# Kernel optimization log

Hardware: AMD Instinct MI355X
Metric: run time of the kernel (lower is better)

Reference implementation:

```python
import jax, jax.numpy as jnp
import numpy as np

N, E = 50000, 800000
F_IN, F_H, H, F_OUT = 128, 16, 8, 64
NEG_SLOPE = 0.2
LN_EPS = 1e-5


def setup_inputs() -> dict:
    key = jax.random.key(0)
    ks = jax.random.split(key, 8)
    g = lambda k, shp, fan: (jax.random.normal(k, shp, jnp.float32) / np.sqrt(fan).astype(np.float32))
    return {
        "x": jax.random.normal(ks[0], (N, F_IN), jnp.float32),
        "edge_index": jax.random.randint(ks[1], (2, E), 0, N, jnp.int32),
        "Wl1": g(ks[2], (F_IN, H * F_H), F_IN),
        "Wr1": g(ks[3], (F_IN, H * F_H), F_IN),
        "att1": g(ks[4], (H, F_H), F_H),
        "bias1": jnp.zeros((H * F_H,), jnp.float32),
        "g1": jnp.ones((H * F_H,), jnp.float32),
        "b1": jnp.zeros((H * F_H,), jnp.float32),
        "Wl2": g(ks[5], (H * F_H, F_OUT), H * F_H),
        "Wr2": g(ks[6], (H * F_H, F_OUT), H * F_H),
        "att2": g(ks[7], (1, F_OUT), F_OUT),
        "bias2": jnp.zeros((F_OUT,), jnp.float32),
        "g2": jnp.ones((F_OUT,), jnp.float32),
        "b2": jnp.zeros((F_OUT,), jnp.float32),
    }


def gatv2_conv(x, edge_index, Wl, Wr, att, bias, concat):
    """PyG GATv2Conv (eval mode, dropout inactive).
    message m_e = leaky_relu(xl[src] + xr[dst]); alpha = softmax_dst(<m_e, att>);
    out_i = sum_{e: dst=i} alpha_e * xl[src_e]. Concat or mean over heads, + bias.
    """
    n = x.shape[0]
    h, c = att.shape
    src, dst = edge_index[0], edge_index[1]
    xl = (x @ Wl).reshape(n, h, c)  # source transform (lin_l)
    xr = (x @ Wr).reshape(n, h, c)  # target transform (lin_r)
    e = jax.nn.leaky_relu(xl[src] + xr[dst], NEG_SLOPE)  # [E,h,c]
    a = jnp.einsum("ehc,hc->eh", e, att)  # [E,h]
    # segment softmax over destination node
    m = jax.ops.segment_max(a, dst, num_segments=n)  # [n,h]
    m = jnp.where(jnp.isfinite(m), m, 0.0)  # isolated nodes -> -inf guard
    ea = jnp.exp(a - m[dst])
    s = jax.ops.segment_sum(ea, dst, num_segments=n)
    alpha = ea / (s[dst] + 1e-16)  # [E,h]
    out = jax.ops.segment_sum(xl[src] * alpha[..., None], dst, num_segments=n)  # [n,h,c]
    out = out.reshape(n, h * c) if concat else out.mean(axis=1)
    return out + bias


def layer_norm(x, gamma, beta):
    mu = x.mean(-1, keepdims=True)
    var = ((x - mu) ** 2).mean(-1, keepdims=True)
    return (x - mu) * jax.lax.rsqrt(var + LN_EPS) * gamma + beta


def reference(x, edge_index, Wl1, Wr1, att1, bias1, g1, b1,
              Wl2, Wr2, att2, bias2, g2, b2):
    h1 = gatv2_conv(x, edge_index, Wl1, Wr1, att1, bias1, concat=True)
    h1 = jax.nn.elu(layer_norm(h1, g1, b1))
    h2 = gatv2_conv(h1, edge_index, Wl2, Wr2, att2, bias2, concat=False)
    return layer_norm(h2, g2, b2)
```

## Files before the change

### kernel.cpp

```cpp
#include <hip/hip_runtime.h>
#include <hip/hip_bf16.h>
#include <math.h>

typedef short s16x8 __attribute__((ext_vector_type(8)));
typedef float f32x4 __attribute__((ext_vector_type(4)));
typedef float f32x2 __attribute__((ext_vector_type(2)));

__device__ __forceinline__ float bflo(unsigned u) { return __uint_as_float(u << 16); }
__device__ __forceinline__ float bfhi(unsigned u) { return __uint_as_float(u & 0xffff0000u); }
__device__ __forceinline__ unsigned short f2bf(float f) {
    __hip_bfloat16 h = __float2bfloat16(f);
    return __builtin_bit_cast(unsigned short, h);
}
__device__ __forceinline__ f32x4 mfma_bf16(s16x8 a, s16x8 b, f32x4 c) {
    asm("v_mfma_f32_16x16x32_bf16 %0, %1, %2, %0" : "+v"(c) : "v"(a), "v"(b));
    return c;
}
__device__ __forceinline__ f32x2 unpk2(unsigned u) { return (f32x2){bflo(u), bfhi(u)}; }
__device__ __forceinline__ f32x2 plrelu(f32x2 x) {
    return __builtin_elementwise_max(x, x * 0.2f);
}
template <int CTRL>
__device__ __forceinline__ float dpp_add(float v) {
    int y = __builtin_amdgcn_update_dpp(0, __builtin_bit_cast(int, v), CTRL, 0xf, 0xf, true);
    return v + __builtin_bit_cast(float, y);
}
__device__ __forceinline__ float red8(float p) {
    p = dpp_add<0xB1>(p); p = dpp_add<0x4E>(p); return dpp_add<0x141>(p);
}
__device__ __forceinline__ float red16(float p) {
    p = dpp_add<0xB1>(p); p = dpp_add<0x4E>(p);
    p = dpp_add<0x141>(p); return dpp_add<0x140>(p);
}

__global__ void prep_kernel(const float* __restrict__ Wl1, const float* __restrict__ Wr1,
                            const float* __restrict__ Wl2, const float* __restrict__ Wr2,
                            unsigned short* __restrict__ Wt1, unsigned short* __restrict__ Wt2,
                            int* __restrict__ deg, int n) {
    int idx = blockIdx.x * 256 + threadIdx.x;
    if (idx < 256 * 128) {
        int c = idx >> 7, k = idx & 127;
        float v = (c < 128) ? Wl1[k * 128 + c] : Wr1[k * 128 + (c - 128)];
        Wt1[idx] = f2bf(v);
    } else if (idx < 256 * 128 + 128 * 128) {
        int j = idx - 256 * 128;
        int c = j >> 7, k = j & 127;
        float v = (c < 64) ? Wl2[k * 64 + c] : Wr2[k * 64 + (c - 64)];
        Wt2[j] = f2bf(v);
    } else {
        int z = idx - (256 * 128 + 128 * 128);
        int i = z * 4;
        if (i + 3 < n) *reinterpret_cast<int4*>(&deg[i]) = make_int4(0, 0, 0, 0);
        else {
            if (i < n) deg[i] = 0;
            if (i + 1 < n) deg[i + 1] = 0;
            if (i + 2 < n) deg[i + 2] = 0;
        }
    }
}

__global__ __launch_bounds__(256) void degree_gemm_kernel(
    const int* __restrict__ dst, int* __restrict__ deg, int* __restrict__ rank, int E,
    int dblocks,
    const float* __restrict__ A, const unsigned short* __restrict__ Wt,
    unsigned short* __restrict__ Cl, unsigned short* __restrict__ Cr, int nrows) {
    __shared__ unsigned short As[64 * 128];
    if (blockIdx.x < (unsigned)dblocks) {
        int e = blockIdx.x * 256 + threadIdx.x;
        if (e < E) rank[e] = atomicAdd(&deg[dst[e]], 1);
        return;
    }
    constexpr int NOUT = 256, HALF = 128, CT = 4;
    int t = threadIdx.x, lane = t & 63, wave = t >> 6;
    int row_base = (blockIdx.x - dblocks) * 64;
    int rows_here = nrows - row_base;
    #pragma unroll
    for (int it = 0; it < 4; ++it) {
        int q = it * 256 + t;
        int r = q >> 4, c8 = q & 15;
        int su = r * 16 + (c8 ^ (r & 7));
        s16x8 v = {0, 0, 0, 0, 0, 0, 0, 0};
        if (r < rows_here) {
            const float4* g = reinterpret_cast<const float4*>(
                A + ((size_t)(row_base + r)) * 128 + c8 * 8);
            float4 v0 = g[0], v1 = g[1];
            union { s16x8 s; unsigned short u[8]; } pk;
            pk.u[0] = f2bf(v0.x); pk.u[1] = f2bf(v0.y);
            pk.u[2] = f2bf(v0.z); pk.u[3] = f2bf(v0.w);
            pk.u[4] = f2bf(v1.x); pk.u[5] = f2bf(v1.y);
            pk.u[6] = f2bf(v1.z); pk.u[7] = f2bf(v1.w);
            v = pk.s;
        }
        reinterpret_cast<s16x8*>(As)[su] = v;
    }
    __syncthreads();
    int m16 = lane & 15, kg = lane >> 4;
    int colw = wave * (NOUT / 4);
    s16x8 bfr[CT][4];
    const s16x8* Wt16 = reinterpret_cast<const s16x8*>(Wt);
    #pragma unroll
    for (int ct = 0; ct < CT; ++ct)
        #pragma unroll
        for (int ks = 0; ks < 4; ++ks)
            bfr[ct][ks] = Wt16[(size_t)(colw + ct * 16 + m16) * 16 + ks * 4 + kg];
    f32x4 acc[4][CT];
    #pragma unroll
    for (int rt = 0; rt < 4; ++rt)
        #pragma unroll
        for (int ct = 0; ct < CT; ++ct) acc[rt][ct] = (f32x4){0.f, 0.f, 0.f, 0.f};
    const s16x8* As16 = reinterpret_cast<const s16x8*>(As);
    int sw = m16 & 7;
    #pragma unroll
    for (int rt = 0; rt < 4; ++rt) {
        int abase = (rt * 16 + m16) * 16;
        #pragma unroll
        for (int ks = 0; ks < 4; ++ks) {
            s16x8 af = As16[abase + ((ks * 4 + kg) ^ sw)];
            #pragma unroll
            for (int ct = 0; ct < CT; ++ct)
                acc[rt][ct] = mfma_bf16(bfr[ct][ks], af, acc[rt][ct]);
        }
    }
    #pragma unroll
    for (int rt = 0; rt < 4; ++rt) {
        int row = row_base + rt * 16 + m16;
        if (row < nrows) {
            #pragma unroll
            for (int ct = 0; ct < CT; ++ct) {
                int n0 = colw + ct * 16 + kg * 4;
                unsigned short* Cp = (n0 < HALF) ? (Cl + n0) : (Cr + (n0 - HALF));
                ushort4 w4;
                w4.x = f2bf(acc[rt][ct][0]);
                w4.y = f2bf(acc[rt][ct][1]);
                w4.z = f2bf(acc[rt][ct][2]);
                w4.w = f2bf(acc[rt][ct][3]);
                *reinterpret_cast<ushort4*>(&Cp[(size_t)row * HALF]) = w4;
            }
        }
    }
}

__global__ __launch_bounds__(1024) void scan_part_kernel(const int* __restrict__ deg,
                                                         int* __restrict__ off,
                                                         int* __restrict__ bsum, int n) {
    __shared__ int wsum[16];
    int t = threadIdx.x, lane = t & 63, w = t >> 6;
    int i = blockIdx.x * 4096 + t * 4;
    int4 v = make_int4(0, 0, 0, 0);
    if (i + 3 < n) v = *reinterpret_cast<const int4*>(&deg[i]);
    else {
        if (i < n) v.x = deg[i];
        if (i + 1 < n) v.y = deg[i + 1];
        if (i + 2 < n) v.z = deg[i + 2];
    }
    int tsum = v.x + v.y + v.z + v.w;
    int x = tsum;
    #pragma unroll
    for (int d = 1; d < 64; d <<= 1) { int y = __shfl_up(x, d); if (lane >= d) x += y; }
    if (lane == 63) wsum[w] = x;
    __syncthreads();
    if (t < 16) {
        int y = wsum[t];
        #pragma unroll
        for (int d = 1; d < 16; d <<= 1) { int z = __shfl_up(y, d); if (t >= d) y += z; }
        wsum[t] = y;
    }
    __syncthreads();
    int excl = ((w == 0) ? 0 : wsum[w - 1]) + (x - tsum);
    if (i < n) off[i] = excl;
    if (i + 1 < n) off[i + 1] = excl + v.x;
    if (i + 2 < n) off[i + 2] = excl + v.x + v.y;
    if (i + 3 < n) off[i + 3] = excl + v.x + v.y + v.z;
    __syncthreads();
    if (t == 1023) bsum[blockIdx.x] = wsum[15];
}

__global__ __launch_bounds__(1024) void scan_add_kernel(int* __restrict__ off,
                                                        const int* __restrict__ bsum,
                                                        int nblk, int n) {
    int b = blockIdx.x;
    int base = 0;
    for (int j = 0; j < b; ++j) base += bsum[j];
    int i = b * 4096 + threadIdx.x * 4;
    if (i + 3 < n) {
        int4 v = *reinterpret_cast<const int4*>(&off[i]);
        v.x += base; v.y += base; v.z += base; v.w += base;
        *reinterpret_cast<int4*>(&off[i]) = v;
    } else {
        if (i < n) off[i] += base;
        if (i + 1 < n) off[i + 1] += base;
        if (i + 2 < n) off[i + 2] += base;
    }
    if (b == 0 && threadIdx.x == 0) {
        int tot = 0;
        for (int j = 0; j < nblk; ++j) tot += bsum[j];
        off[n] = tot;
    }
}

__global__ void scatter_kernel(const int* __restrict__ src, const int* __restrict__ dst,
                               const int* __restrict__ off, const int* __restrict__ rank,
                               int* __restrict__ ssrc, int E) {
    int e = blockIdx.x * blockDim.x + threadIdx.x;
    if (e < E) {
        int d = dst[e];
        ssrc[off[d] + rank[e]] = src[e];
    }
}

__global__ __launch_bounds__(256) void mfma_gemm128_kernel(
    const unsigned short* __restrict__ A, const unsigned short* __restrict__ Wt,
    unsigned short* __restrict__ Cl, unsigned short* __restrict__ Cr, int nrows) {
    constexpr int NOUT = 128, HALF = 64, CT = 2;
    __shared__ unsigned short As[64 * 128];
    int t = threadIdx.x, lane = t & 63, wave = t >> 6;
    int row_base = blockIdx.x * 64;
    int rows_here = nrows - row_base;
    #pragma unroll
    for (int it = 0; it < 4; ++it) {
        int q = it * 256 + t;
        int r = q >> 4, c8 = q & 15;
        int su = r * 16 + (c8 ^ (r & 7));
        s16x8 v = {0, 0, 0, 0, 0, 0, 0, 0};
        if (r < rows_here)
            v = *reinterpret_cast<const s16x8*>(A + ((size_t)(row_base + r)) * 128 + c8 * 8);
        reinterpret_cast<s16x8*>(As)[su] = v;
    }
    __syncthreads();
    int m16 = lane & 15, kg = lane >> 4;
    int colw = wave * (NOUT / 4);
    s16x8 bfr[CT][4];
    const s16x8* Wt16 = reinterpret_cast<const s16x8*>(Wt);
    #pragma unroll
    for (int ct = 0; ct < CT; ++ct)
        #pragma unroll
        for (int ks = 0; ks < 4; ++ks)
            bfr[ct][ks] = Wt16[(size_t)(colw + ct * 16 + m16) * 16 + ks * 4 + kg];
    f32x4 acc[4][CT];
    #pragma unroll
    for (int rt = 0; rt < 4; ++rt)
        #pragma unroll
        for (int ct = 0; ct < CT; ++ct) acc[rt][ct] = (f32x4){0.f, 0.f, 0.f, 0.f};
    const s16x8* As16 = reinterpret_cast<const s16x8*>(As);
    int sw = m16 & 7;
    #pragma unroll
    for (int rt = 0; rt < 4; ++rt) {
        int abase = (rt * 16 + m16) * 16;
        #pragma unroll
        for (int ks = 0; ks < 4; ++ks) {
            s16x8 af = As16[abase + ((ks * 4 + kg) ^ sw)];
            #pragma unroll
            for (int ct = 0; ct < CT; ++ct)
                acc[rt][ct] = mfma_bf16(bfr[ct][ks], af, acc[rt][ct]);
        }
    }
    #pragma unroll
    for (int rt = 0; rt < 4; ++rt) {
        int row = row_base + rt * 16 + m16;
        if (row < nrows) {
            #pragma unroll
            for (int ct = 0; ct < CT; ++ct) {
                int n0 = colw + ct * 16 + kg * 4;
                unsigned short* Cp = (n0 < HALF) ? (Cl + n0) : (Cr + (n0 - HALF));
                ushort4 w4;
                w4.x = f2bf(acc[rt][ct][0]);
                w4.y = f2bf(acc[rt][ct][1]);
                w4.z = f2bf(acc[rt][ct][2]);
                w4.w = f2bf(acc[rt][ct][3]);
                *reinterpret_cast<ushort4*>(&Cp[(size_t)row * HALF]) = w4;
            }
        }
    }
}

__global__ __launch_bounds__(64) void gat1_kernel(
    const unsigned short* __restrict__ xl, const unsigned short* __restrict__ xr,
    const int* __restrict__ off, const int* __restrict__ ssrc,
    const float* __restrict__ att, const float* __restrict__ bias,
    const float* __restrict__ gamma, const float* __restrict__ beta,
    unsigned short* __restrict__ out, int n) {
    int lane = threadIdx.x;
    int node = blockIdx.x;
    if (node >= n) return;
    int h = lane >> 3;
    int i0 = h * 16 + ((lane & 7) << 1);
    f32x2 xrp = unpk2(*reinterpret_cast<const unsigned*>(xr + (size_t)node * 128 + i0));
    f32x2 atp = {att[i0], att[i0 + 1]};
    float s = 0.f;
    f32x2 ac = {0.f, 0.f};
    int beg = off[node], end = off[node + 1];
    int i = beg;
    for (; i + 4 <= end; i += 4) {
        int e0 = ssrc[i], e1 = ssrc[i + 1], e2 = ssrc[i + 2], e3 = ssrc[i + 3];
        unsigned u0 = *reinterpret_cast<const unsigned*>(xl + (size_t)e0 * 128 + i0);
        unsigned u1 = *reinterpret_cast<const unsigned*>(xl + (size_t)e1 * 128 + i0);
        unsigned u2 = *reinterpret_cast<const unsigned*>(xl + (size_t)e2 * 128 + i0);
        unsigned u3 = *reinterpret_cast<const unsigned*>(xl + (size_t)e3 * 128 + i0);
        f32x2 x0 = unpk2(u0), x1 = unpk2(u1), x2 = unpk2(u2), x3 = unpk2(u3);
        f32x2 q0 = plrelu(x0 + xrp) * atp;
        f32x2 q1 = plrelu(x1 + xrp) * atp;
        f32x2 q2 = plrelu(x2 + xrp) * atp;
        f32x2 q3 = plrelu(x3 + xrp) * atp;
        float p0 = q0.x + q0.y, p1 = q1.x + q1.y;
        float p2 = q2.x + q2.y, p3 = q3.x + q3.y;
        p0 = dpp_add<0xB1>(p0); p1 = dpp_add<0xB1>(p1);
        p2 = dpp_add<0xB1>(p2); p3 = dpp_add<0xB1>(p3);
        p0 = dpp_add<0x4E>(p0); p1 = dpp_add<0x4E>(p1);
        p2 = dpp_add<0x4E>(p2); p3 = dpp_add<0x4E>(p3);
        p0 = dpp_add<0x141>(p0); p1 = dpp_add<0x141>(p1);
        p2 = dpp_add<0x141>(p2); p3 = dpp_add<0x141>(p3);
        float w0 = __expf(fminf(p0, 60.f));
        float w1 = __expf(fminf(p1, 60.f));
        float w2 = __expf(fminf(p2, 60.f));
        float w3 = __expf(fminf(p3, 60.f));
        s += (w0 + w1) + (w2 + w3);
        ac += w0 * x0 + w1 * x1;
        ac += w2 * x2 + w3 * x3;
    }
    for (; i < end; ++i) {
        int e = ssrc[i];
        f32x2 xv = unpk2(*reinterpret_cast<const unsigned*>(xl + (size_t)e * 128 + i0));
        f32x2 q = plrelu(xv + xrp) * atp;
        float p = red8(q.x + q.y);
        float w = __expf(fminf(p, 60.f));
        s += w; ac += w * xv;
    }
    float inv = 1.f / (s + 1e-16f);
    float o0 = ac.x * inv + bias[i0];
    float o1 = ac.y * inv + bias[i0 + 1];
    float tsum = o0 + o1;
    #pragma unroll
    for (int d = 1; d < 64; d <<= 1) tsum += __shfl_xor(tsum, d);
    float mu = tsum * (1.f / 128.f);
    float d0 = o0 - mu, d1 = o1 - mu;
    float vsum = d0 * d0 + d1 * d1;
    #pragma unroll
    for (int d = 1; d < 64; d <<= 1) vsum += __shfl_xor(vsum, d);
    float rs = rsqrtf(vsum * (1.f / 128.f) + 1e-5f);
    float y0 = d0 * rs * gamma[i0] + beta[i0];
    float y1 = d1 * rs * gamma[i0 + 1] + beta[i0 + 1];
    y0 = y0 > 0.f ? y0 : expm1f(y0);
    y1 = y1 > 0.f ? y1 : expm1f(y1);
    unsigned pk = (unsigned)f2bf(y0) | ((unsigned)f2bf(y1) << 16);
    *reinterpret_cast<unsigned*>(out + (size_t)node * 128 + i0) = pk;
}

__global__ __launch_bounds__(64) void gat2_kernel(
    const unsigned short* __restrict__ xl, const unsigned short* __restrict__ xr,
    const int* __restrict__ off, const int* __restrict__ ssrc,
    const float* __restrict__ att, const float* __restrict__ bias,
    const float* __restrict__ gamma, const float* __restrict__ beta,
    float* __restrict__ out, int n) {
    int lane = threadIdx.x;
    int node = blockIdx.x;
    if (node >= n) return;
    int j2 = lane >> 4;
    int q = lane & 15;
    int fb = q * 4;
    uint2 uxr = *reinterpret_cast<const uint2*>(xr + (size_t)node * 64 + fb);
    f32x2 xr0 = unpk2(uxr.x), xr1 = unpk2(uxr.y);
    float4 at = *reinterpret_cast<const float4*>(att + fb);
    f32x2 at0 = {at.x, at.y}, at1 = {at.z, at.w};
    float s = 0.f;
    f32x2 ac0 = {0.f, 0.f}, ac1 = {0.f, 0.f};
    int beg = off[node], end = off[node + 1];
    for (int base = beg; base < end; base += 4) {
        int idx = base + j2;
        bool valid = idx < end;
        int e = ssrc[valid ? idx : beg];
        uint2 u = *reinterpret_cast<const uint2*>(xl + (size_t)e * 64 + fb);
        f32x2 x0 = unpk2(u.x), x1 = unpk2(u.y);
        f32x2 g0 = plrelu(x0 + xr0) * at0;
        f32x2 g1 = plrelu(x1 + xr1) * at1;
        f32x2 gs = g0 + g1;
        float p = red16(gs.x + gs.y);
        float w = valid ? __expf(fminf(p, 60.f)) : 0.f;
        s += w;
        ac0 += w * x0;
        ac1 += w * x1;
    }
    #pragma unroll
    for (int d = 16; d <= 32; d <<= 1) {
        s += __shfl_xor(s, d);
        ac0.x += __shfl_xor(ac0.x, d); ac0.y += __shfl_xor(ac0.y, d);
        ac1.x += __shfl_xor(ac1.x, d); ac1.y += __shfl_xor(ac1.y, d);
    }
    float inv = 1.f / (s + 1e-16f);
    float4 bi = *reinterpret_cast<const float4*>(bias + fb);
    float o0 = ac0.x * inv + bi.x;
    float o1 = ac0.y * inv + bi.y;
    float o2 = ac1.x * inv + bi.z;
    float o3 = ac1.y * inv + bi.w;
    float tsum = red16((o0 + o1) + (o2 + o3));
    float mu = tsum * (1.f / 64.f);
    float d0 = o0 - mu, d1 = o1 - mu, d2 = o2 - mu, d3 = o3 - mu;
    float vs = red16((d0 * d0 + d1 * d1) + (d2 * d2 + d3 * d3));
    float rs = rsqrtf(vs * (1.f / 64.f) + 1e-5f);
    if (j2 == 0) {
        float4 ga = *reinterpret_cast<const float4*>(gamma + fb);
        float4 be = *reinterpret_cast<const float4*>(beta + fb);
        float4 y;
        y.x = d0 * rs * ga.x + be.x;
        y.y = d1 * rs * ga.y + be.y;
        y.z = d2 * rs * ga.z + be.z;
        y.w = d3 * rs * ga.w + be.w;
        *reinterpret_cast<float4*>(out + (size_t)node * 64 + fb) = y;
    }
}

extern "C" void kernel_launch(void* const* d_in, const int* in_sizes, int n_in,
                              void* d_out, int out_size, void* d_ws, size_t ws_size,
                              hipStream_t stream) {
    const float* x = (const float*)d_in[0];
    const int* ei = (const int*)d_in[1];
    const float* Wl1 = (const float*)d_in[2];
    const float* Wr1 = (const float*)d_in[3];
    const float* att1 = (const float*)d_in[4];
    const float* bias1 = (const float*)d_in[5];
    const float* g1 = (const float*)d_in[6];
    const float* b1 = (const float*)d_in[7];
    const float* Wl2 = (const float*)d_in[8];
    const float* Wr2 = (const float*)d_in[9];
    const float* att2 = (const float*)d_in[10];
    const float* bias2 = (const float*)d_in[11];
    const float* g2 = (const float*)d_in[12];
    const float* b2 = (const float*)d_in[13];
    float* out = (float*)d_out;

    const int N = in_sizes[0] / 128;
    const int E = in_sizes[1] / 2;
    const int* src = ei;
    const int* dstp = ei + E;

    char* p = (char*)d_ws;
    auto alloc = [&](size_t bytes) -> char* {
        char* r = p;
        p += (bytes + 255) & ~(size_t)255;
        return r;
    };
    int* deg = (int*)alloc((size_t)N * 4);
    int* rank = (int*)alloc((size_t)E * 4);
    int* off = (int*)alloc((size_t)(N + 1) * 4);
    int* ssrc = (int*)alloc((size_t)E * 4);
    int* bsum = (int*)alloc(64 * 4);
    unsigned short* Wt1 = (unsigned short*)alloc(256 * 128 * 2);
    unsigned short* Wt2 = (unsigned short*)alloc(128 * 128 * 2);
    unsigned short* bufA = (unsigned short*)alloc((size_t)N * 128 * 2);
    unsigned short* bufB = (unsigned short*)alloc((size_t)N * 128 * 2);
    unsigned short* h1u = (unsigned short*)alloc((size_t)N * 128 * 2);

    const int nblk = (N + 4095) / 4096;
    const int gblocks = (N + 63) / 64;
    const int dblocks = (E + 255) / 256;
    const int prep_threads = 256 * 128 + 128 * 128 + (N + 3) / 4;

    prep_kernel<<<(prep_threads + 255) / 256, 256, 0, stream>>>(
        Wl1, Wr1, Wl2, Wr2, Wt1, Wt2, deg, N);
    degree_gemm_kernel<<<dblocks + gblocks, 256, 0, stream>>>(
        dstp, deg, rank, E, dblocks, x, Wt1, bufA, bufB, N);
    scan_part_kernel<<<nblk, 1024, 0, stream>>>(deg, off, bsum, N);
    scan_add_kernel<<<nblk, 1024, 0, stream>>>(off, bsum, nblk, N);
    scatter_kernel<<<(E + 255) / 256, 256, 0, stream>>>(src, dstp, off, rank, ssrc, E);
    gat1_kernel<<<N, 64, 0, stream>>>(bufA, bufB, off, ssrc, att1, bias1, g1, b1, h1u, N);
    mfma_gemm128_kernel<<<gblocks, 256, 0, stream>>>(h1u, Wt2, bufA, bufB, N);
    gat2_kernel<<<N, 64, 0, stream>>>(bufA, bufB, off, ssrc, att2, bias2, g2, b2, out, N);
}
```

Before: 252.9 us.

## Fuse layer-1 GAT aggregation with layer-2 MFMA projection via shared memory

```diff
diff --git a/kernel.cpp b/kernel.cpp
--- a/kernel.cpp
+++ b/kernel.cpp
@@ -208,141 +208,119 @@
     }
 }
 
-__global__ __launch_bounds__(256) void mfma_gemm128_kernel(
-    const unsigned short* __restrict__ A, const unsigned short* __restrict__ Wt,
-    unsigned short* __restrict__ Cl, unsigned short* __restrict__ Cr, int nrows) {
-    constexpr int NOUT = 128, HALF = 64, CT = 2;
-    __shared__ unsigned short As[64 * 128];
-    int t = threadIdx.x, lane = t & 63, wave = t >> 6;
-    int row_base = blockIdx.x * 64;
-    int rows_here = nrows - row_base;
-    #pragma unroll
-    for (int it = 0; it < 4; ++it) {
-        int q = it * 256 + t;
-        int r = q >> 4, c8 = q & 15;
-        int su = r * 16 + (c8 ^ (r & 7));
-        s16x8 v = {0, 0, 0, 0, 0, 0, 0, 0};
-        if (r < rows_here)
-            v = *reinterpret_cast<const s16x8*>(A + ((size_t)(row_base + r)) * 128 + c8 * 8);
-        reinterpret_cast<s16x8*>(As)[su] = v;
-    }
-    __syncthreads();
-    int m16 = lane & 15, kg = lane >> 4;
-    int colw = wave * (NOUT / 4);
-    s16x8 bfr[CT][4];
-    const s16x8* Wt16 = reinterpret_cast<const s16x8*>(Wt);
-    #pragma unroll
-    for (int ct = 0; ct < CT; ++ct)
-        #pragma unroll
-        for (int ks = 0; ks < 4; ++ks)
-            bfr[ct][ks] = Wt16[(size_t)(colw + ct * 16 + m16) * 16 + ks * 4 + kg];
-    f32x4 acc[4][CT];
-    #pragma unroll
-    for (int rt = 0; rt < 4; ++rt)
-        #pragma unroll
-        for (int ct = 0; ct < CT; ++ct) acc[rt][ct] = (f32x4){0.f, 0.f, 0.f, 0.f};
-    const s16x8* As16 = reinterpret_cast<const s16x8*>(As);
-    int sw = m16 & 7;
-    #pragma unroll
-    for (int rt = 0; rt < 4; ++rt) {
-        int abase = (rt * 16 + m16) * 16;
-        #pragma unroll
-        for (int ks = 0; ks < 4; ++ks) {
-            s16x8 af = As16[abase + ((ks * 4 + kg) ^ sw)];
-            #pragma unroll
-            for (int ct = 0; ct < CT; ++ct)
-                acc[rt][ct] = mfma_bf16(bfr[ct][ks], af, acc[rt][ct]);
-        }
-    }
-    #pragma unroll
-    for (int rt = 0; rt < 4; ++rt) {
-        int row = row_base + rt * 16 + m16;
-        if (row < nrows) {
-            #pragma unroll
-            for (int ct = 0; ct < CT; ++ct) {
-                int n0 = colw + ct * 16 + kg * 4;
-                unsigned short* Cp = (n0 < HALF) ? (Cl + n0) : (Cr + (n0 - HALF));
-                ushort4 w4;
-                w4.x = f2bf(acc[rt][ct][0]);
-                w4.y = f2bf(acc[rt][ct][1]);
-                w4.z = f2bf(acc[rt][ct][2]);
-                w4.w = f2bf(acc[rt][ct][3]);
-                *reinterpret_cast<ushort4*>(&Cp[(size_t)row * HALF]) = w4;
-            }
-        }
-    }
-}
-
-__global__ __launch_bounds__(64) void gat1_kernel(
+__global__ __launch_bounds__(256) void gat1_fused_kernel(
     const unsigned short* __restrict__ xl, const unsigned short* __restrict__ xr,
     const int* __restrict__ off, const int* __restrict__ ssrc,
     const float* __restrict__ att, const float* __restrict__ bias,
     const float* __restrict__ gamma, const float* __restrict__ beta,
-    unsigned short* __restrict__ out, int n) {
-    int lane = threadIdx.x;
-    int node = blockIdx.x;
-    if (node >= n) return;
+    const unsigned short* __restrict__ Wt2,
+    unsigned short* __restrict__ Cl, unsigned short* __restrict__ Cr, int n) {
+    __shared__ unsigned short Ys[16 * 128];
+    int t = threadIdx.x, lane = t & 63, wave = t >> 6;
+    int base = blockIdx.x * 16;
     int h = lane >> 3;
     int i0 = h * 16 + ((lane & 7) << 1);
-    f32x2 xrp = unpk2(*reinterpret_cast<const unsigned*>(xr + (size_t)node * 128 + i0));
-    f32x2 atp = {att[i0], att[i0 + 1]};
-    float s = 0.f;
-    f32x2 ac = {0.f, 0.f};
-    int beg = off[node], end = off[node + 1];
-    int i = beg;
-    for (; i + 4 <= end; i += 4) {
-        int e0 = ssrc[i], e1 = ssrc[i + 1], e2 = ssrc[i + 2], e3 = ssrc[i + 3];
-        unsigned u0 = *reinterpret_cast<const unsigned*>(xl + (size_t)e0 * 128 + i0);
-        unsigned u1 = *reinterpret_cast<const unsigned*>(xl + (size_t)e1 * 128 + i0);
-        unsigned u2 = *reinterpret_cast<const unsigned*>(xl + (size_t)e2 * 128 + i0);
-        unsigned u3 = *reinterpret_cast<const unsigned*>(xl + (size_t)e3 * 128 + i0);
-        f32x2 x0 = unpk2(u0), x1 = unpk2(u1), x2 = unpk2(u2), x3 = unpk2(u3);
-        f32x2 q0 = plrelu(x0 + xrp) * atp;
-        f32x2 q1 = plrelu(x1 + xrp) * atp;
-        f32x2 q2 = plrelu(x2 + xrp) * atp;
-        f32x2 q3 = plrelu(x3 + xrp) * atp;
-        float p0 = q0.x + q0.y, p1 = q1.x + q1.y;
-        float p2 = q2.x + q2.y, p3 = q3.x + q3.y;
-        p0 = dpp_add<0xB1>(p0); p1 = dpp_add<0xB1>(p1);
-        p2 = dpp_add<0xB1>(p2); p3 = dpp_add<0xB1>(p3);
-        p0 = dpp_add<0x4E>(p0); p1 = dpp_add<0x4E>(p1);
-        p2 = dpp_add<0x4E>(p2); p3 = dpp_add<0x4E>(p3);
-        p0 = dpp_add<0x141>(p0); p1 = dpp_add<0x141>(p1);
-        p2 = dpp_add<0x141>(p2); p3 = dpp_add<0x141>(p3);
-        float w0 = __expf(fminf(p0, 60.f));
-        float w1 = __expf(fminf(p1, 60.f));
-        float w2 = __expf(fminf(p2, 60.f));
-        float w3 = __expf(fminf(p3, 60.f));
-        s += (w0 + w1) + (w2 + w3);
-        ac += w0 * x0 + w1 * x1;
-        ac += w2 * x2 + w3 * x3;
-    }
-    for (; i < end; ++i) {
-        int e = ssrc[i];
-        f32x2 xv = unpk2(*reinterpret_cast<const unsigned*>(xl + (size_t)e * 128 + i0));
-        f32x2 q = plrelu(xv + xrp) * atp;
-        float p = red8(q.x + q.y);
-        float w = __expf(fminf(p, 60.f));
-        s += w; ac += w * xv;
-    }
-    float inv = 1.f / (s + 1e-16f);
-    float o0 = ac.x * inv + bias[i0];
-    float o1 = ac.y * inv + bias[i0 + 1];
-    float tsum = o0 + o1;
-    #pragma unroll
-    for (int d = 1; d < 64; d <<= 1) tsum += __shfl_xor(tsum, d);
-    float mu = tsum * (1.f / 128.f);
-    float d0 = o0 - mu, d1 = o1 - mu;
-    float vsum = d0 * d0 + d1 * d1;
-    #pragma unroll
-    for (int d = 1; d < 64; d <<= 1) vsum += __shfl_xor(vsum, d);
-    float rs = rsqrtf(vsum * (1.f / 128.f) + 1e-5f);
-    float y0 = d0 * rs * gamma[i0] + beta[i0];
-    float y1 = d1 * rs * gamma[i0 + 1] + beta[i0 + 1];
-    y0 = y0 > 0.f ? y0 : expm1f(y0);
-    y1 = y1 > 0.f ? y1 : expm1f(y1);
-    unsigned pk = (unsigned)f2bf(y0) | ((unsigned)f2bf(y1) << 16);
-    *reinterpret_cast<unsigned*>(out + (size_t)node * 128 + i0) = pk;
+    int u16 = i0 >> 3;
+    int dw = (i0 & 7) >> 1;
+    for (int q = 0; q < 4; ++q) {
+        int slot = wave * 4 + q;
+        int node = base + slot;
+        unsigned pk = 0;
+        if (node < n) {
+            f32x2 xrp = unpk2(*reinterpret_cast<const unsigned*>(xr + (size_t)node * 128 + i0));
+            f32x2 atp = {att[i0], att[i0 + 1]};
+            float s = 0.f;
+            f32x2 ac = {0.f, 0.f};
+            int beg = off[node], end = off[node + 1];
+            int i = beg;
+            for (; i + 4 <= end; i += 4) {
+                int e0 = ssrc[i], e1 = ssrc[i + 1], e2 = ssrc[i + 2], e3 = ssrc[i + 3];
+                unsigned u0 = *reinterpret_cast<const unsigned*>(xl + (size_t)e0 * 128 + i0);
+                unsigned u1 = *reinterpret_cast<const unsigned*>(xl + (size_t)e1 * 128 + i0);
+                unsigned u2 = *reinterpret_cast<const unsigned*>(xl + (size_t)e2 * 128 + i0);
+                unsigned u3 = *reinterpret_cast<const unsigned*>(xl + (size_t)e3 * 128 + i0);
+                f32x2 x0 = unpk2(u0), x1 = unpk2(u1), x2 = unpk2(u2), x3 = unpk2(u3);
+                f32x2 q0 = plrelu(x0 + xrp) * atp;
+                f32x2 q1 = plrelu(x1 + xrp) * atp;
+                f32x2 q2 = plrelu(x2 + xrp) * atp;
+                f32x2 q3 = plrelu(x3 + xrp) * atp;
+                float p0 = q0.x + q0.y, p1 = q1.x + q1.y;
+                float p2 = q2.x + q2.y, p3 = q3.x + q3.y;
+                p0 = dpp_add<0xB1>(p0); p1 = dpp_add<0xB1>(p1);
+                p2 = dpp_add<0xB1>(p2); p3 = dpp_add<0xB1>(p3);
+                p0 = dpp_add<0x4E>(p0); p1 = dpp_add<0x4E>(p1);
+                p2 = dpp_add<0x4E>(p2); p3 = dpp_add<0x4E>(p3);
+                p0 = dpp_add<0x141>(p0); p1 = dpp_add<0x141>(p1);
+                p2 = dpp_add<0x141>(p2); p3 = dpp_add<0x141>(p3);
+                float w0 = __expf(fminf(p0, 60.f));
+                float w1 = __expf(fminf(p1, 60.f));
+                float w2 = __expf(fminf(p2, 60.f));
+                float w3 = __expf(fminf(p3, 60.f));
+                s += (w0 + w1) + (w2 + w3);
+                ac += w0 * x0 + w1 * x1;
+                ac += w2 * x2 + w3 * x3;
+            }
+            for (; i < end; ++i) {
+                int e = ssrc[i];
+                f32x2 xv = unpk2(*reinterpret_cast<const unsigned*>(xl + (size_t)e * 128 + i0));
+                f32x2 qv = plrelu(xv + xrp) * atp;
+                float p = red8(qv.x + qv.y);
+                float w = __expf(fminf(p, 60.f));
+                s += w; ac += w * xv;
+            }
+            float inv = 1.f / (s + 1e-16f);
+            float o0 = ac.x * inv + bias[i0];
+            float o1 = ac.y * inv + bias[i0 + 1];
+            float tsum = o0 + o1;
+            #pragma unroll
+            for (int d = 1; d < 64; d <<= 1) tsum += __shfl_xor(tsum, d);
+            float mu = tsum * (1.f / 128.f);
+            float d0 = o0 - mu, d1 = o1 - mu;
+            float vsum = d0 * d0 + d1 * d1;
+            #pragma unroll
+            for (int d = 1; d < 64; d <<= 1) vsum += __shfl_xor(vsum, d);
+            float rs = rsqrtf(vsum * (1.f / 128.f) + 1e-5f);
+            float y0 = d0 * rs * gamma[i0] + beta[i0];
+            float y1 = d1 * rs * gamma[i0 + 1] + beta[i0 + 1];
+            y0 = y0 > 0.f ? y0 : expm1f(y0);
+            y1 = y1 > 0.f ? y1 : expm1f(y1);
+            pk = (unsigned)f2bf(y0) | ((unsigned)f2bf(y1) << 16);
+        }
+        int su = u16 ^ (slot & 7);
+        *reinterpret_cast<unsigned*>(&Ys[(slot * 16 + su) * 8 + dw * 2]) = pk;
+    }
+    __syncthreads();
+    int m16 = lane & 15, kg = lane >> 4;
+    int colw = wave * 32;
+    const s16x8* Wt16 = reinterpret_cast<const s16x8*>(Wt2);
+    const s16x8* As16 = reinterpret_cast<const s16x8*>(Ys);
+    int sw = m16 & 7;
+    f32x4 acc[2];
+    acc[0] = (f32x4){0.f, 0.f, 0.f, 0.f};
+    acc[1] = (f32x4){0.f, 0.f, 0.f, 0.f};
+    #pragma unroll
+    for (int ks = 0; ks < 4; ++ks) {
+        s16x8 af = As16[m16 * 16 + ((ks * 4 + kg) ^ sw)];
+        #pragma unroll
+        for (int ct = 0; ct < 2; ++ct) {
+            s16x8 bf = Wt16[(size_t)(colw + ct * 16 + m16) * 16 + ks * 4 + kg];
+            acc[ct] = mfma_bf16(bf, af, acc[ct]);
+        }
+    }
+    int row = base + m16;
+    if (row < n) {
+        #pragma unroll
+        for (int ct = 0; ct < 2; ++ct) {
+            int n0 = colw + ct * 16 + kg * 4;
+            unsigned short* Cp = (n0 < 64) ? (Cl + n0) : (Cr + (n0 - 64));
+            ushort4 w4;
+            w4.x = f2bf(acc[ct][0]);
+            w4.y = f2bf(acc[ct][1]);
+            w4.z = f2bf(acc[ct][2]);
+            w4.w = f2bf(acc[ct][3]);
+            *reinterpret_cast<ushort4*>(&Cp[(size_t)row * 64]) = w4;
+        }
+    }
 }
 
 __global__ __launch_bounds__(64) void gat2_kernel(
@@ -447,7 +425,8 @@
     unsigned short* Wt2 = (unsigned short*)alloc(128 * 128 * 2);
     unsigned short* bufA = (unsigned short*)alloc((size_t)N * 128 * 2);
     unsigned short* bufB = (unsigned short*)alloc((size_t)N * 128 * 2);
-    unsigned short* h1u = (unsigned short*)alloc((size_t)N * 128 * 2);
+    unsigned short* bufC = (unsigned short*)alloc((size_t)N * 64 * 2);
+    unsigned short* bufD = (unsigned short*)alloc((size_t)N * 64 * 2);
 
     const int nblk = (N + 4095) / 4096;
     const int gblocks = (N + 63) / 64;
@@ -461,7 +440,7 @@
     scan_part_kernel<<<nblk, 1024, 0, stream>>>(deg, off, bsum, N);
     scan_add_kernel<<<nblk, 1024, 0, stream>>>(off, bsum, nblk, N);
     scatter_kernel<<<(E + 255) / 256, 256, 0, stream>>>(src, dstp, off, rank, ssrc, E);
-    gat1_kernel<<<N, 64, 0, stream>>>(bufA, bufB, off, ssrc, att1, bias1, g1, b1, h1u, N);
-    mfma_gemm128_kernel<<<gblocks, 256, 0, stream>>>(h1u, Wt2, bufA, bufB, N);
-    gat2_kernel<<<N, 64, 0, stream>>>(bufA, bufB, off, ssrc, att2, bias2, g2, b2, out, N);
-}
+    gat1_fused_kernel<<<(N + 15) / 16, 256, 0, stream>>>(
+        bufA, bufB, off, ssrc, att1, bias1, g1, b1, Wt2, bufC, bufD, N);
+    gat2_kernel<<<N, 64, 0, stream>>>(bufC, bufD, off, ssrc, att2, bias2, g2, b2, out, N);
+}
```

After: 264.6 us. 4.6% more time.

## Split degree counters into four sub-buckets to reduce atomic contention

Applied to the files above, without the earlier changes.

```diff
diff --git a/kernel.cpp b/kernel.cpp
--- a/kernel.cpp
+++ b/kernel.cpp
@@ -36,7 +36,7 @@
 __global__ void prep_kernel(const float* __restrict__ Wl1, const float* __restrict__ Wr1,
                             const float* __restrict__ Wl2, const float* __restrict__ Wr2,
                             unsigned short* __restrict__ Wt1, unsigned short* __restrict__ Wt2,
-                            int* __restrict__ deg, int n) {
+                            int* __restrict__ deg4, int n4) {
     int idx = blockIdx.x * 256 + threadIdx.x;
     if (idx < 256 * 128) {
         int c = idx >> 7, k = idx & 127;
@@ -50,24 +50,24 @@
     } else {
         int z = idx - (256 * 128 + 128 * 128);
         int i = z * 4;
-        if (i + 3 < n) *reinterpret_cast<int4*>(&deg[i]) = make_int4(0, 0, 0, 0);
+        if (i + 3 < n4) *reinterpret_cast<int4*>(&deg4[i]) = make_int4(0, 0, 0, 0);
         else {
-            if (i < n) deg[i] = 0;
-            if (i + 1 < n) deg[i + 1] = 0;
-            if (i + 2 < n) deg[i + 2] = 0;
+            if (i < n4) deg4[i] = 0;
+            if (i + 1 < n4) deg4[i + 1] = 0;
+            if (i + 2 < n4) deg4[i + 2] = 0;
         }
     }
 }
 
 __global__ __launch_bounds__(256) void degree_gemm_kernel(
-    const int* __restrict__ dst, int* __restrict__ deg, int* __restrict__ rank, int E,
-    int dblocks,
+    const int* __restrict__ dst, int* __restrict__ deg4, int* __restrict__ rank, int E,
+    int N, int dblocks,
     const float* __restrict__ A, const unsigned short* __restrict__ Wt,
     unsigned short* __restrict__ Cl, unsigned short* __restrict__ Cr, int nrows) {
     __shared__ unsigned short As[64 * 128];
     if (blockIdx.x < (unsigned)dblocks) {
         int e = blockIdx.x * 256 + threadIdx.x;
-        if (e < E) rank[e] = atomicAdd(&deg[dst[e]], 1);
+        if (e < E) rank[e] = atomicAdd(&deg4[(e & 3) * N + dst[e]], 1);
         return;
     }
     constexpr int NOUT = 256, HALF = 128, CT = 4;
@@ -140,19 +140,37 @@
     }
 }
 
-__global__ __launch_bounds__(1024) void scan_part_kernel(const int* __restrict__ deg,
+__global__ __launch_bounds__(1024) void scan_part_kernel(const int* __restrict__ deg4,
                                                          int* __restrict__ off,
-                                                         int* __restrict__ bsum, int n) {
+                                                         int4* __restrict__ sbase,
+                                                         int* __restrict__ bsum,
+                                                         int n, int N) {
     __shared__ int wsum[16];
     int t = threadIdx.x, lane = t & 63, w = t >> 6;
     int i = blockIdx.x * 4096 + t * 4;
-    int4 v = make_int4(0, 0, 0, 0);
-    if (i + 3 < n) v = *reinterpret_cast<const int4*>(&deg[i]);
-    else {
-        if (i < n) v.x = deg[i];
-        if (i + 1 < n) v.y = deg[i + 1];
-        if (i + 2 < n) v.z = deg[i + 2];
-    }
+    int4 A0 = make_int4(0, 0, 0, 0), A1 = A0, A2 = A0, A3 = A0;
+    if (i + 3 < n) {
+        A0 = *reinterpret_cast<const int4*>(&deg4[0 * N + i]);
+        A1 = *reinterpret_cast<const int4*>(&deg4[1 * N + i]);
+        A2 = *reinterpret_cast<const int4*>(&deg4[2 * N + i]);
+        A3 = *reinterpret_cast<const int4*>(&deg4[3 * N + i]);
+    } else {
+        int* a0 = &A0.x; int* a1 = &A1.x; int* a2 = &A2.x; int* a3 = &A3.x;
+        for (int j = 0; j < 4; ++j) {
+            if (i + j < n) {
+                a0[j] = deg4[0 * N + i + j];
+                a1[j] = deg4[1 * N + i + j];
+                a2[j] = deg4[2 * N + i + j];
+                a3[j] = deg4[3 * N + i + j];
+            }
+        }
+    }
+    int4 v = make_int4(A0.x + A1.x + A2.x + A3.x, A0.y + A1.y + A2.y + A3.y,
+                       A0.z + A1.z + A2.z + A3.z, A0.w + A1.w + A2.w + A3.w);
+    if (i < n) sbase[i] = make_int4(0, A0.x, A0.x + A1.x, A0.x + A1.x + A2.x);
+    if (i + 1 < n) sbase[i + 1] = make_int4(0, A0.y, A0.y + A1.y, A0.y + A1.y + A2.y);
+    if (i + 2 < n) sbase[i + 2] = make_int4(0, A0.z, A0.z + A1.z, A0.z + A1.z + A2.z);
+    if (i + 3 < n) sbase[i + 3] = make_int4(0, A0.w, A0.w + A1.w, A0.w + A1.w + A2.w);
     int tsum = v.x + v.y + v.z + v.w;
     int x = tsum;
     #pragma unroll
@@ -176,20 +194,28 @@
 }
 
 __global__ __launch_bounds__(1024) void scan_add_kernel(int* __restrict__ off,
+                                                        int4* __restrict__ sbase,
                                                         const int* __restrict__ bsum,
                                                         int nblk, int n) {
     int b = blockIdx.x;
     int base = 0;
     for (int j = 0; j < b; ++j) base += bsum[j];
     int i = b * 4096 + threadIdx.x * 4;
+    int o[4];
     if (i + 3 < n) {
         int4 v = *reinterpret_cast<const int4*>(&off[i]);
-        v.x += base; v.y += base; v.z += base; v.w += base;
-        *reinterpret_cast<int4*>(&off[i]) = v;
+        o[0] = v.x + base; o[1] = v.y + base; o[2] = v.z + base; o[3] = v.w + base;
+        *reinterpret_cast<int4*>(&off[i]) = make_int4(o[0], o[1], o[2], o[3]);
     } else {
-        if (i < n) off[i] += base;
-        if (i + 1 < n) off[i + 1] += base;
-        if (i + 2 < n) off[i + 2] += base;
+        for (int j = 0; j < 4; ++j)
+            if (i + j < n) { o[j] = off[i + j] + base; off[i + j] = o[j]; }
+    }
+    #pragma unroll
+    for (int j = 0; j < 4; ++j) {
+        if (i + j < n) {
+            int4 s = sbase[i + j];
+            sbase[i + j] = make_int4(s.x + o[j], s.y + o[j], s.z + o[j], s.w + o[j]);
+        }
     }
     if (b == 0 && threadIdx.x == 0) {
         int tot = 0;
@@ -199,12 +225,13 @@
 }
 
 __global__ void scatter_kernel(const int* __restrict__ src, const int* __restrict__ dst,
-                               const int* __restrict__ off, const int* __restrict__ rank,
+                               const int* __restrict__ abase, const int* __restrict__ rank,
                                int* __restrict__ ssrc, int E) {
     int e = blockIdx.x * blockDim.x + threadIdx.x;
     if (e < E) {
         int d = dst[e];
-        ssrc[off[d] + rank[e]] = src[e];
+        int pos = abase[4 * d + (e & 3)] + rank[e];
+        ssrc[pos] = src[e];
     }
 }
 
@@ -259,7 +286,7 @@
         int row = row_base + rt * 16 + m16;
         if (row < nrows) {
             #pragma unroll
-            for (int ct = 0; ct < CT; ++ct) {
+            for (int ct = 0; ct < 2; ++ct) {
                 int n0 = colw + ct * 16 + kg * 4;
                 unsigned short* Cp = (n0 < HALF) ? (Cl + n0) : (Cr + (n0 - HALF));
                 ushort4 w4;
@@ -438,9 +465,10 @@
         p += (bytes + 255) & ~(size_t)255;
         return r;
     };
-    int* deg = (int*)alloc((size_t)N * 4);
+    int* deg4 = (int*)alloc((size_t)N * 4 * 4);
     int* rank = (int*)alloc((size_t)E * 4);
     int* off = (int*)alloc((size_t)(N + 1) * 4);
+    int4* sbase = (int4*)alloc((size_t)N * 16);
     int* ssrc = (int*)alloc((size_t)E * 4);
     int* bsum = (int*)alloc(64 * 4);
     unsigned short* Wt1 = (unsigned short*)alloc(256 * 128 * 2);
@@ -452,15 +480,17 @@
     const int nblk = (N + 4095) / 4096;
     const int gblocks = (N + 63) / 64;
     const int dblocks = (E + 255) / 256;
-    const int prep_threads = 256 * 128 + 128 * 128 + (N + 3) / 4;
+    const int n4 = N * 4;
+    const int prep_threads = 256 * 128 + 128 * 128 + (n4 + 3) / 4;
 
     prep_kernel<<<(prep_threads + 255) / 256, 256, 0, stream>>>(
-        Wl1, Wr1, Wl2, Wr2, Wt1, Wt2, deg, N);
+        Wl1, Wr1, Wl2, Wr2, Wt1, Wt2, deg4, n4);
     degree_gemm_kernel<<<dblocks + gblocks, 256, 0, stream>>>(
-        dstp, deg, rank, E, dblocks, x, Wt1, bufA, bufB, N);
-    scan_part_kernel<<<nblk, 1024, 0, stream>>>(deg, off, bsum, N);
-    scan_add_kernel<<<nblk, 1024, 0, stream>>>(off, bsum, nblk, N);
-    scatter_kernel<<<(E + 255) / 256, 256, 0, stream>>>(src, dstp, off, rank, ssrc, E);
+        dstp, deg4, rank, E, N, dblocks, x, Wt1, bufA, bufB, N);
+    scan_part_kernel<<<nblk, 1024, 0, stream>>>(deg4, off, sbase, bsum, N, N);
+    scan_add_kernel<<<nblk, 1024, 0, stream>>>(off, sbase, bsum, nblk, N);
+    scatter_kernel<<<(E + 255) / 256, 256, 0, stream>>>(src, dstp, (const int*)sbase, rank,
+                                                        ssrc, E);
     gat1_kernel<<<N, 64, 0, stream>>>(bufA, bufB, off, ssrc, att1, bias1, g1, b1, h1u, N);
     mfma_gemm128_kernel<<<gblocks, 256, 0, stream>>>(h1u, Wt2, bufA, bufB, N);
     gat2_kernel<<<N, 64, 0, stream>>>(bufA, bufB, off, ssrc, att2, bias2, g2, b2, out, N);
```

Result: no change. 255.5 us (+1.0%).

## Build CSR via two-level bucket partition instead of atomic degree, scan and scatter

Applied to the files above, without the earlier changes.

```diff
diff --git a/kernel.cpp b/kernel.cpp
--- a/kernel.cpp
+++ b/kernel.cpp
@@ -33,10 +33,12 @@
     p = dpp_add<0x141>(p); return dpp_add<0x140>(p);
 }
 
+#define EPB 2048
+#define BSTRIDE 8192
+
 __global__ void prep_kernel(const float* __restrict__ Wl1, const float* __restrict__ Wr1,
                             const float* __restrict__ Wl2, const float* __restrict__ Wr2,
-                            unsigned short* __restrict__ Wt1, unsigned short* __restrict__ Wt2,
-                            int* __restrict__ deg, int n) {
+                            unsigned short* __restrict__ Wt1, unsigned short* __restrict__ Wt2) {
     int idx = blockIdx.x * 256 + threadIdx.x;
     if (idx < 256 * 128) {
         int c = idx >> 7, k = idx & 127;
@@ -47,32 +49,59 @@
         int c = j >> 7, k = j & 127;
         float v = (c < 64) ? Wl2[k * 64 + c] : Wr2[k * 64 + (c - 64)];
         Wt2[j] = f2bf(v);
-    } else {
-        int z = idx - (256 * 128 + 128 * 128);
-        int i = z * 4;
-        if (i + 3 < n) *reinterpret_cast<int4*>(&deg[i]) = make_int4(0, 0, 0, 0);
-        else {
-            if (i < n) deg[i] = 0;
-            if (i + 1 < n) deg[i + 1] = 0;
-            if (i + 2 < n) deg[i + 2] = 0;
-        }
-    }
-}
-
-__global__ __launch_bounds__(256) void degree_gemm_kernel(
-    const int* __restrict__ dst, int* __restrict__ deg, int* __restrict__ rank, int E,
-    int dblocks,
+    }
+}
+
+__global__ __launch_bounds__(256) void part_gemm_kernel(
+    const int* __restrict__ src, const int* __restrict__ dst, int* __restrict__ cnt,
+    int* __restrict__ bucketbuf, int E, int NB, int pblocks,
     const float* __restrict__ A, const unsigned short* __restrict__ Wt,
     unsigned short* __restrict__ Cl, unsigned short* __restrict__ Cr, int nrows) {
-    __shared__ unsigned short As[64 * 128];
-    if (blockIdx.x < (unsigned)dblocks) {
-        int e = blockIdx.x * 256 + threadIdx.x;
-        if (e < E) rank[e] = atomicAdd(&deg[dst[e]], 1);
+    __shared__ char smem[19456];
+    int t = threadIdx.x;
+    if (blockIdx.x < (unsigned)pblocks) {
+        int* sdst = (int*)smem;
+        int* ssl = (int*)(smem + 8192);
+        int* hist = (int*)(smem + 16384);
+        int* gbase = (int*)(smem + 17408);
+        int* cursor = (int*)(smem + 18432);
+        int e0 = blockIdx.x * EPB;
+        #pragma unroll
+        for (int it = 0; it < EPB / 256; ++it) {
+            int i = it * 256 + t;
+            int e = e0 + i;
+            sdst[i] = (e < E) ? dst[e] : -1;
+            ssl[i] = (e < E) ? src[e] : 0;
+        }
+        if (t < NB) hist[t] = 0;
+        __syncthreads();
+        #pragma unroll
+        for (int it = 0; it < EPB / 256; ++it) {
+            int d = sdst[it * 256 + t];
+            if (d >= 0) atomicAdd(&hist[d >> 8], 1);
+        }
+        __syncthreads();
+        if (t < NB) {
+            gbase[t] = atomicAdd(&cnt[t], hist[t]);
+            cursor[t] = 0;
+        }
+        __syncthreads();
+        #pragma unroll
+        for (int it = 0; it < EPB / 256; ++it) {
+            int i = it * 256 + t;
+            int d = sdst[i];
+            if (d >= 0) {
+                int b = d >> 8;
+                int l = atomicAdd(&cursor[b], 1);
+                bucketbuf[b * BSTRIDE + gbase[b] + l] = ((d & 255) << 16) | ssl[i];
+            }
+        }
         return;
     }
+    unsigned short* As = (unsigned short*)smem;
     constexpr int NOUT = 256, HALF = 128, CT = 4;
-    int t = threadIdx.x, lane = t & 63, wave = t >> 6;
-    int row_base = (blockIdx.x - dblocks) * 64;
+    int lane = t & 63, wave = t >> 6;
+    int row_base = (blockIdx.x - pblocks) * 64;
     int rows_here = nrows - row_base;
     #pragma unroll
     for (int it = 0; it < 4; ++it) {
@@ -140,71 +169,53 @@
     }
 }
 
-__global__ __launch_bounds__(1024) void scan_part_kernel(const int* __restrict__ deg,
-                                                         int* __restrict__ off,
-                                                         int* __restrict__ bsum, int n) {
-    __shared__ int wsum[16];
-    int t = threadIdx.x, lane = t & 63, w = t >> 6;
-    int i = blockIdx.x * 4096 + t * 4;
-    int4 v = make_int4(0, 0, 0, 0);
-    if (i + 3 < n) v = *reinterpret_cast<const int4*>(&deg[i]);
-    else {
-        if (i < n) v.x = deg[i];
-        if (i + 1 < n) v.y = deg[i + 1];
-        if (i + 2 < n) v.z = deg[i + 2];
-    }
-    int tsum = v.x + v.y + v.z + v.w;
-    int x = tsum;
-    #pragma unroll
-    for (int d = 1; d < 64; d <<= 1) { int y = __shfl_up(x, d); if (lane >= d) x += y; }
-    if (lane == 63) wsum[w] = x;
-    __syncthreads();
-    if (t < 16) {
-        int y = wsum[t];
-        #pragma unroll
-        for (int d = 1; d < 16; d <<= 1) { int z = __shfl_up(y, d); if (t >= d) y += z; }
-        wsum[t] = y;
-    }
-    __syncthreads();
-    int excl = ((w == 0) ? 0 : wsum[w - 1]) + (x - tsum);
-    if (i < n) off[i] = excl;
-    if (i + 1 < n) off[i + 1] = excl + v.x;
-    if (i + 2 < n) off[i + 2] = excl + v.x + v.y;
-    if (i + 3 < n) off[i + 3] = excl + v.x + v.y + v.z;
-    __syncthreads();
-    if (t == 1023) bsum[blockIdx.x] = wsum[15];
-}
-
-__global__ __launch_bounds__(1024) void scan_add_kernel(int* __restrict__ off,
-                                                        const int* __restrict__ bsum,
-                                                        int nblk, int n) {
-    int b = blockIdx.x;
-    int base = 0;
-    for (int j = 0; j < b; ++j) base += bsum[j];
-    int i = b * 4096 + threadIdx.x * 4;
-    if (i + 3 < n) {
-        int4 v = *reinterpret_cast<const int4*>(&off[i]);
-        v.x += base; v.y += base; v.z += base; v.w += base;
-        *reinterpret_cast<int4*>(&off[i]) = v;
-    } else {
-        if (i < n) off[i] += base;
-        if (i + 1 < n) off[i + 1] += base;
-        if (i + 2 < n) off[i + 2] += base;
-    }
-    if (b == 0 && threadIdx.x == 0) {
-        int tot = 0;
-        for (int j = 0; j < nblk; ++j) tot += bsum[j];
-        off[n] = tot;
-    }
-}
-
-__global__ void scatter_kernel(const int* __restrict__ src, const int* __restrict__ dst,
-                               const int* __restrict__ off, const int* __restrict__ rank,
-                               int* __restrict__ ssrc, int E) {
-    int e = blockIdx.x * blockDim.x + threadIdx.x;
-    if (e < E) {
-        int d = dst[e];
-        ssrc[off[d] + rank[e]] = src[e];
+__global__ __launch_bounds__(256) void bucket_csr_kernel(
+    const int* __restrict__ cnt, const int* __restrict__ bucketbuf,
+    int* __restrict__ off, int* __restrict__ ssrc, int N, int NB, int E) {
+    __shared__ int nhist[256];
+    __shared__ int ncur[256];
+    __shared__ int wred[4];
+    int b = blockIdx.x, t = threadIdx.x;
+    int lane = t & 63, wv = t >> 6;
+    int v = (t < b && t < NB) ? cnt[t] : 0;
+    float vf = __int_as_float(v);
+    (void)vf;
+    int x = v;
+    #pragma unroll
+    for (int d = 1; d < 64; d <<= 1) x += __shfl_xor(x, d);
+    if (lane == 0) wred[wv] = x;
+    __syncthreads();
+    int ebase = wred[0] + wred[1] + wred[2] + wred[3];
+    int ne = cnt[b];
+    int nb0 = b << 8;
+    int nn = min(256, N - nb0);
+    nhist[t] = 0;
+    __syncthreads();
+    const int* bb = bucketbuf + (size_t)b * BSTRIDE;
+    for (int i = t; i < ne; i += 256) {
+        int p = bb[i];
+        atomicAdd(&nhist[p >> 16], 1);
+    }
+    __syncthreads();
+    int h = nhist[t];
+    int sx = h;
+    #pragma unroll
+    for (int d = 1; d < 64; d <<= 1) { int y = __shfl_up(sx, d); if (lane >= d) sx += y; }
+    if (lane == 63) wred[wv] = sx;
+    __syncthreads();
+    int woff = 0;
+    #pragma unroll
+    for (int j = 0; j < 4; ++j) woff += (j < wv) ? wred[j] : 0;
+    int excl = woff + sx - h;
+    if (t < nn) off[nb0 + t] = ebase + excl;
+    ncur[t] = excl;
+    if (b == NB - 1 && t == 0) off[N] = ebase + ne;
+    __syncthreads();
+    for (int i = t; i < ne; i += 256) {
+        int p = bb[i];
+        int nl = p >> 16;
+        int l = atomicAdd(&ncur[nl], 1);
+        ssrc[ebase + l] = p & 0xFFFF;
     }
 }
 
@@ -259,7 +270,7 @@
         int row = row_base + rt * 16 + m16;
         if (row < nrows) {
             #pragma unroll
-            for (int ct = 0; ct < CT; ++ct) {
+            for (int ct = 0; ct < 2; ++ct) {
                 int n0 = colw + ct * 16 + kg * 4;
                 unsigned short* Cp = (n0 < HALF) ? (Cl + n0) : (Cr + (n0 - HALF));
                 ushort4 w4;
@@ -431,6 +442,7 @@
     const int E = in_sizes[1] / 2;
     const int* src = ei;
     const int* dstp = ei + E;
+    const int NB = (N + 255) >> 8;
 
     char* p = (char*)d_ws;
     auto alloc = [&](size_t bytes) -> char* {
@@ -438,29 +450,25 @@
         p += (bytes + 255) & ~(size_t)255;
         return r;
     };
-    int* deg = (int*)alloc((size_t)N * 4);
-    int* rank = (int*)alloc((size_t)E * 4);
+    int* cnt = (int*)alloc(256 * 4);
+    int* bucketbuf = (int*)alloc((size_t)NB * BSTRIDE * 4);
     int* off = (int*)alloc((size_t)(N + 1) * 4);
     int* ssrc = (int*)alloc((size_t)E * 4);
-    int* bsum = (int*)alloc(64 * 4);
     unsigned short* Wt1 = (unsigned short*)alloc(256 * 128 * 2);
     unsigned short* Wt2 = (unsigned short*)alloc(128 * 128 * 2);
     unsigned short* bufA = (unsigned short*)alloc((size_t)N * 128 * 2);
     unsigned short* bufB = (unsigned short*)alloc((size_t)N * 128 * 2);
     unsigned short* h1u = (unsigned short*)alloc((size_t)N * 128 * 2);
 
-    const int nblk = (N + 4095) / 4096;
     const int gblocks = (N + 63) / 64;
-    const int dblocks = (E + 255) / 256;
-    const int prep_threads = 256 * 128 + 128 * 128 + (N + 3) / 4;
-
-    prep_kernel<<<(prep_threads + 255) / 256, 256, 0, stream>>>(
-        Wl1, Wr1, Wl2, Wr2, Wt1, Wt2, deg, N);
-    degree_gemm_kernel<<<dblocks + gblocks, 256, 0, stream>>>(
-        dstp, deg, rank, E, dblocks, x, Wt1, bufA, bufB, N);
-    scan_part_kernel<<<nblk, 1024, 0, stream>>>(deg, off, bsum, N);
-    scan_add_kernel<<<nblk, 1024, 0, stream>>>(off, bsum, nblk, N);
-    scatter_kernel<<<(E + 255) / 256, 256, 0, stream>>>(src, dstp, off, rank, ssrc, E);
+    const int pblocks = (E + EPB - 1) / EPB;
+
+    hipMemsetAsync(cnt, 0, 256 * 4, stream);
+    prep_kernel<<<(256 * 128 + 128 * 128 + 255) / 256, 256, 0, stream>>>(
+        Wl1, Wr1, Wl2, Wr2, Wt1, Wt2);
+    part_gemm_kernel<<<pblocks + gblocks, 256, 0, stream>>>(
+        src, dstp, cnt, bucketbuf, E, NB, pblocks, x, Wt1, bufA, bufB, N);
+    bucket_csr_kernel<<<NB, 256, 0, stream>>>(cnt, bucketbuf, off, ssrc, N, NB, E);
     gat1_kernel<<<N, 64, 0, stream>>>(bufA, bufB, off, ssrc, att1, bias1, g1, b1, h1u, N);
     mfma_gemm128_kernel<<<gblocks, 256, 0, stream>>>(h1u, Wt2, bufA, bufB, N);
     gat2_kernel<<<N, 64, 0, stream>>>(bufA, bufB, off, ssrc, att2, bias2, g2, b2, out, N);
```

Result: faster. 225.7 us (-10.8%).
